# Kernel optimization log

Measured on AMD Instinct MI355X. Metric: run time of the kernel, lower is better.

## Reference

```python
import jax, jax.numpy as jnp
import numpy as np
import math

N_SAMPLES = 15


def sample_match(P, n_samples=N_SAMPLES):
    """Greedy argmax matching with row/col suppression, vectorized over batch.
    P: [B, N, M] (non-negative softmax scores). Returns (rows, cols): [B, S] int32.
    Matches torch: idx = (P == P.max()).nonzero()[0] -> first (row-major) argmax.
    """
    B, N, M = P.shape
    row_ids = jnp.arange(N)
    col_ids = jnp.arange(M)

    def step(P, _):
        flat_idx = jnp.argmax(P.reshape(B, N * M), axis=1)  # first max, row-major
        row = flat_idx // M  # [B]
        col = flat_idx % M   # [B]
        # suppress chosen row and column: P[row,:]=0 ; P[:,col]=0
        mask = (row_ids[None, :, None] == row[:, None, None]) | (
            col_ids[None, None, :] == col[:, None, None])  # [B,N,M]
        P = jnp.where(mask, jnp.zeros((), P.dtype), P)
        return P, (row, col)

    _, (rows, cols) = jax.lax.scan(step, P, None, length=n_samples)
    return rows.T, cols.T  # [B, S]


def setup_inputs() -> dict:
    key = jax.random.key(0)
    k1, k2, k3, k4 = jax.random.split(key, 4)
    B, D, N = 16, 512, 2048
    return {
        "src_embedding": jax.random.normal(k1, (B, D, N), dtype=jnp.float32),
        "tgt_embedding": jax.random.normal(k2, (B, D, N), dtype=jnp.float32),
        "src": jax.random.normal(k3, (B, N, 3), dtype=jnp.float32),
        "tgt": jax.random.normal(k4, (B, N, 3), dtype=jnp.float32),
    }


def reference(src_embedding, tgt_embedding, src, tgt):
    # input_shape == 'bnc': permute point clouds to [B, 3, N]
    src = jnp.swapaxes(src, 1, 2)
    tgt = jnp.swapaxes(tgt, 1, 2)
    B = src.shape[0]
    d_k = src_embedding.shape[1]

    # scores[b, s, t] = softmax_t( <src_emb[b,:,s], tgt_emb[b,:,t]> / sqrt(d_k) )
    logits = jnp.einsum('bds,bdt->bst', src_embedding, tgt_embedding) / math.sqrt(d_k)
    scores = jax.nn.softmax(logits, axis=2)

    # greedy one-to-one matching on detached scores
    rows, cols = sample_match(jax.lax.stop_gradient(scores))  # [B, S]

    # gather matched points: [B, 3, S]
    topk_src = jnp.take_along_axis(src, rows[:, None, :], axis=2)
    topk_tgt = jnp.take_along_axis(tgt, cols[:, None, :], axis=2)

    src_c = topk_src - topk_src.mean(axis=2, keepdims=True)
    tgt_c = topk_tgt - topk_tgt.mean(axis=2, keepdims=True)
    H = jnp.einsum('bis,bjs->bij', src_c, tgt_c)  # [B, 3, 3]

    u, s, vh = jnp.linalg.svd(H)
    v = jnp.swapaxes(vh, -1, -2)  # torch.svd returns V, jnp returns V^H
    ut = jnp.swapaxes(u, -1, -2)
    r = v @ ut
    det = jnp.linalg.det(r)
    reflect = jnp.array([1.0, 1.0, -1.0], dtype=H.dtype)  # diag(1,1,-1) right-mult
    r_fix = (v * reflect[None, None, :]) @ ut
    R = jnp.where((det < 0)[:, None, None], r_fix, r)  # [B, 3, 3]

    # soft correspondence: src_corr = tgt @ scores^T  -> [B, 3, N_src]
    src_corr = jnp.einsum('bjt,bst->bjs', tgt, scores)
    t = jnp.einsum('bij,bj->bi', -R, src.mean(axis=2)) + src_corr.mean(axis=2)
    return R, t.reshape(B, 3)
```

## Files before the change

kernel.cpp:

```cpp
#include <hip/hip_runtime.h>
#include <hip/hip_fp16.h>
#include <math.h>

typedef unsigned short u16;
typedef __attribute__((ext_vector_type(8))) short bf16x8;
typedef __attribute__((ext_vector_type(4))) float f32x4;

constexpr int B_ = 16;
constexpr int D_ = 512;
constexpr int N_ = 2048;
constexpr int S_ = 15;
constexpr int TOPK = 16;

constexpr int BK  = 32;
constexpr int KP  = 2 * D_;
constexpr int SCW = 132;
constexpr int BN7 = 256;
constexpr int NCH7 = N_ / BN7;

__device__ __forceinline__ void gl_lds16(const void* g, void* s) {
    __builtin_amdgcn_global_load_lds(
        (const __attribute__((address_space(1))) unsigned int*)g,
        (__attribute__((address_space(3))) unsigned int*)s, 16, 0, 0);
}

__device__ __forceinline__ unsigned enc1(float x) {
    x = fminf(x, 448.f);
    unsigned u = __float_as_uint(x);
    if (u < 0x3C800000u) return 0u;
    unsigned r = u + 0x7FFFFu + ((u >> 20) & 1u);
    unsigned f = (r >> 20) - 0x3C0u;
    return f > 0x7Eu ? 0x7Eu : f;
}
__device__ __forceinline__ float dec1(unsigned f) {
    return f ? __uint_as_float((f + 0x3C0u) << 20) : 0.f;
}

__global__ __launch_bounds__(256) void packbf(
    const float* __restrict__ srcE, const float* __restrict__ tgtE,
    u16* __restrict__ srcP, u16* __restrict__ tgtP)
{
    const int t = threadIdx.x;
    const int b = blockIdx.z & 15, sel = blockIdx.z >> 4;
    const float* in = (sel ? tgtE : srcE) + (size_t)b * D_ * N_;
    u16* out = (sel ? tgtP : srcP) + (size_t)b * N_ * KP;
    const int n0 = blockIdx.x * 64, k0 = blockIdx.y * 64;

    __shared__ float T[64][69];

    #pragma unroll
    for (int it = 0; it < 4; it++) {
        int r = it * 16 + (t >> 4);
        int c = (t & 15) * 4;
        float4 v = *(const float4*)&in[(size_t)(k0 + r) * N_ + n0 + c];
        T[c + 0][r] = v.x; T[c + 1][r] = v.y; T[c + 2][r] = v.z; T[c + 3][r] = v.w;
    }
    __syncthreads();

    const int nn = t >> 2, kc = (t & 3) * 16;
    __align__(16) u16 hi[16], lo[16];
    #pragma unroll
    for (int j = 0; j < 16; j++) {
        float x = T[nn][kc + j];
        unsigned u = __float_as_uint(x);
        unsigned hr = u + 0x7fff + ((u >> 16) & 1);
        u16 h = (u16)(hr >> 16);
        float hf = __uint_as_float((unsigned)h << 16);
        float xl = x - hf;
        unsigned ul = __float_as_uint(xl);
        unsigned lr = ul + 0x7fff + ((ul >> 16) & 1);
        hi[j] = h; lo[j] = (u16)(lr >> 16);
    }
    u16* op = out + (size_t)(n0 + nn) * KP + k0 + kc;
    *(int4*)op         = *(int4*)hi;  *(int4*)(op + 8)   = *(int4*)(hi + 8);
    *(int4*)(op + 512) = *(int4*)lo;  *(int4*)(op + 520) = *(int4*)(lo + 8);
}

__global__ __launch_bounds__(512, 2) void gemm7(
    const u16* __restrict__ srcP, const u16* __restrict__ tgtP,
    float* __restrict__ rzbuf, float* __restrict__ topv, int* __restrict__ topc,
    unsigned char* __restrict__ e8)
{
    __shared__ __align__(16) u16 sS[2 * 16384];
    __shared__ __align__(16) float sC[128 * SCW];

    const int tid = threadIdx.x;
    const int w = tid >> 6, lane = tid & 63;
    const int wr = w >> 2, wc = w & 3;
    const int sr = lane >> 2, q = lane & 3;
    const int bid = blockIdx.x;
    const int swz = (bid & 7) * 32 + (bid >> 3);
    const int b  = swz >> 4;
    const int s0 = (swz & 15) * 128;
    const float scale = 0.044194173824159216f;

    const u16* srcPb = srcP + (size_t)b * N_ * KP;
    const u16* tgtPb = tgtP + (size_t)b * N_ * KP;

    const int sls = ((lane & 3) ^ ((lane >> 3) & 3)) * 8;
    const u16* pAh = srcPb + (size_t)(s0 + w * 16 + (lane >> 2)) * KP + sls;
    const u16* pB  = tgtPb + (size_t)(w * 16 + (lane >> 2)) * KP + sls;
    const int aro = (lane & 15) * BK + (((lane >> 4) ^ ((lane >> 1) & 3)) * 8);

    auto stage = [&](int bi, int s, int c0) {
        u16* base = &sS[bi * 16384];
        const int t32 = (s & 15) * BK;
        gl_lds16(pAh + t32, base + w * 512);
        if (s < 16) {
            gl_lds16(pAh + 512 + t32, base + 4096 + w * 512);
            gl_lds16(pB + (size_t)c0 * KP + t32,         base + 8192 + w * 512);
            gl_lds16(pB + (size_t)(c0 + 128) * KP + t32, base + 12288 + w * 512);
        } else {
            gl_lds16(pB + (size_t)c0 * KP + 512 + t32,         base + 8192 + w * 512);
            gl_lds16(pB + (size_t)(c0 + 128) * KP + 512 + t32, base + 12288 + w * 512);
        }
    };

    float z_loc = 0.f;
    float tv[TOPK]; int tc16[TOPK];
    #pragma unroll
    for (int k = 0; k < TOPK; k++) { tv[k] = -1e30f; tc16[k] = 0x7fffffff; }

    stage(0, 0, 0);

    for (int ch = 0; ch < NCH7; ch++) {
        const int c0 = ch * BN7;
        f32x4 acc[4][4];
        #pragma unroll
        for (int i = 0; i < 4; i++)
            #pragma unroll
            for (int j = 0; j < 4; j++) acc[i][j] = (f32x4){0.f, 0.f, 0.f, 0.f};

        for (int s = 0; s < 32; s++) {
            __syncthreads();
            if (s < 31)              stage((s + 1) & 1, s + 1, c0);
            else if (ch < NCH7 - 1)  stage(0, 0, c0 + BN7);
            const u16* base = &sS[(s & 1) * 16384];
            bf16x8 afr[4], bfr[4];
            #pragma unroll
            for (int j = 0; j < 4; j++)
                bfr[j] = *(const bf16x8*)&base[8192 + wc * 2048 + j * 512 + aro];
            #pragma unroll
            for (int i = 0; i < 4; i++)
                afr[i] = *(const bf16x8*)&base[wr * 2048 + i * 512 + aro];
            #pragma unroll
            for (int i = 0; i < 4; i++)
                #pragma unroll
                for (int j = 0; j < 4; j++)
                    acc[i][j] = __builtin_amdgcn_mfma_f32_16x16x32_bf16(
                        afr[i], bfr[j], acc[i][j], 0, 0, 0);
            if (s < 16) {
                #pragma unroll
                for (int i = 0; i < 4; i++)
                    afr[i] = *(const bf16x8*)&base[4096 + wr * 2048 + i * 512 + aro];
                #pragma unroll
                for (int i = 0; i < 4; i++)
                    #pragma unroll
                    for (int j = 0; j < 4; j++)
                        acc[i][j] = __builtin_amdgcn_mfma_f32_16x16x32_bf16(
                            afr[i], bfr[j], acc[i][j], 0, 0, 0);
            }
        }

        #pragma unroll 1
        for (int h = 0; h < 2; h++) {
            __syncthreads();
            if ((wc >> 1) == h) {
                const int cb = (wc & 1) * 64;
                #pragma unroll
                for (int i = 0; i < 4; i++)
                    #pragma unroll
                    for (int j = 0; j < 4; j++)
                        #pragma unroll
                        for (int r = 0; r < 4; r++)
                            sC[(wr * 64 + i * 16 + (lane >> 4) * 4 + r) * SCW
                               + cb + j * 16 + (lane & 15)] = acc[i][j][r] * scale;
            }
            __syncthreads();
            const float* rowp = &sC[(w * 16 + sr) * SCW + q * 32];
            const int cbase = c0 + h * 128 + q * 32;
            const size_t erow = ((size_t)(b * N_ + s0 + w * 16 + sr)) * N_
                                + c0 + h * 128 + q * 32;
            #pragma unroll 1
            for (int mo = 0; mo < 2; mo++) {
                unsigned ow0 = 0, ow1 = 0, ow2 = 0, ow3 = 0;
                #pragma unroll
                for (int mi = 0; mi < 4; mi++) {
                    float4 v4 = *(const float4*)&rowp[mo * 16 + mi * 4];
                    const float vv[4] = {v4.x, v4.y, v4.z, v4.w};
                    unsigned wb = 0;
                    #pragma unroll
                    for (int e = 0; e < 4; e++) {
                        float v = vv[e];
                        float ex = __expf(v);
                        z_loc += ex;
                        wb |= enc1(ex) << (8 * e);
                        if (v > tv[15]) {
                            const int c = cbase + mo * 16 + mi * 4 + e;
                            #pragma unroll
                            for (int k = 15; k >= 1; k--) {
                                bool bk  = v > tv[k];
                                bool bk1 = v > tv[k - 1];
                                float sv = bk1 ? tv[k - 1] : v;
                                int   sc = bk1 ? tc16[k - 1] : c;
                                tv[k]   = bk ? sv : tv[k];
                                tc16[k] = bk ? sc : tc16[k];
                            }
                            if (v > tv[0]) { tv[0] = v; tc16[0] = c; }
                        }
                    }
                    if (mi == 0) ow0 = wb; else if (mi == 1) ow1 = wb;
                    else if (mi == 2) ow2 = wb; else ow3 = wb;
                }
                if (e8) *(uint4*)&e8[erow + mo * 16] = make_uint4(ow0, ow1, ow2, ow3);
            }
        }
    }

    float* sCw = &sC[w * 16 * SCW];
    int*   cbw = (int*)sCw;
    float* vbw = sCw + 1024;
    float* zqw = sCw + 2048;
    zqw[lane] = z_loc;
    #pragma unroll
    for (int k = 0; k < TOPK; k++) {
        vbw[lane * 16 + k] = tv[k];
        cbw[lane * 16 + k] = tc16[k];
    }
    if (q == 0) {
        float Z = zqw[lane] + zqw[lane + 1] + zqw[lane + 2] + zqw[lane + 3];
        float lz = logf(Z);
        const int grow = s0 + w * 16 + sr;
        rzbuf[b * N_ + grow] = 1.0f / Z;
        float tmin = -1e30f; int tminslot = 0, tmincol = 0x7fffffff;
        #pragma unroll
        for (int k = 0; k < TOPK; k++) { tv[k] = -1e30f; tc16[k] = 0x7fffffff; }
        for (int qq = 0; qq < 4; qq++) {
            #pragma unroll 1
            for (int k = 0; k < TOPK; k++) {
                float v = vbw[(lane + qq) * 16 + k];
                int c = cbw[(lane + qq) * 16 + k];
                bool ins = (v > tmin) || (v == tmin && c < tmincol);
                if (ins) {
                    #pragma unroll
                    for (int k2 = 0; k2 < TOPK; k2++)
                        if (k2 == tminslot) { tv[k2] = v; tc16[k2] = c; }
                    tmin = tv[0]; tmincol = tc16[0]; tminslot = 0;
                    #pragma unroll
                    for (int k2 = 1; k2 < TOPK; k2++) {
                        bool worse = (tv[k2] < tmin) || (tv[k2] == tmin && tc16[k2] > tmincol);
                        if (worse) { tmin = tv[k2]; tmincol = tc16[k2]; tminslot = k2; }
                    }
                }
            }
        }
        unsigned used = 0;
        size_t rowbase = ((size_t)b * N_ + grow) * TOPK;
        for (int o = 0; o < TOPK; o++) {
            float bvv = -1e31f; int bcc = 0x7fffffff; int bk = 0;
            #pragma unroll
            for (int k = 0; k < TOPK; k++) {
                bool u = (used >> k) & 1u;
                bool better = !u && ((tv[k] > bvv) || (tv[k] == bvv && tc16[k] < bcc));
                if (better) { bvv = tv[k]; bcc = tc16[k]; bk = k; }
            }
            used |= 1u << bk;
            topv[rowbase + o] = bvv - lz;
            topc[rowbase + o] = bcc;
        }
    }
}

__global__ __launch_bounds__(256) void colsum3(
    const unsigned char* __restrict__ e8, const float* __restrict__ rzbuf,
    float* __restrict__ colsum)
{
    const int b = blockIdx.z, s0 = blockIdx.y * 128, t0 = blockIdx.x * 1024;
    __shared__ float srz[128];
    if (threadIdx.x < 128) srz[threadIdx.x] = rzbuf[b * N_ + s0 + threadIdx.x];
    __syncthreads();
    const int t = t0 + threadIdx.x * 4;
    const unsigned char* p = e8 + ((size_t)(b * N_ + s0)) * N_ + t;
    float a0 = 0.f, a1 = 0.f, a2 = 0.f, a3 = 0.f;
    #pragma unroll 4
    for (int s = 0; s < 128; s++) {
        unsigned v = *(const unsigned*)(p + (size_t)s * N_);
        float r = srz[s];
        a0 += dec1(v & 255u) * r;
        a1 += dec1((v >> 8) & 255u) * r;
        a2 += dec1((v >> 16) & 255u) * r;
        a3 += dec1(v >> 24) * r;
    }
    atomicAdd(&colsum[b * N_ + t + 0], a0);
    atomicAdd(&colsum[b * N_ + t + 1], a1);
    atomicAdd(&colsum[b * N_ + t + 2], a2);
    atomicAdd(&colsum[b * N_ + t + 3], a3);
}

__global__ __launch_bounds__(512, 2) void gemm8(
    const u16* __restrict__ srcP, const u16* __restrict__ tgtP,
    const float* __restrict__ rzbuf, float* __restrict__ colsum)
{
    __shared__ __align__(16) u16 sS[2 * 16384];
    __shared__ float sRZ[128];

    const int tid = threadIdx.x;
    const int w = tid >> 6, lane = tid & 63;
    const int wr = w >> 2, wc = w & 3;
    const int bid = blockIdx.x;
    const int swz = (bid & 7) * 64 + (bid >> 3);
    const int b   = swz >> 5;
    const int rb  = swz & 31;
    const int s0  = (rb & 15) * 128;
    const int cb0 = (rb >> 4) * 1024;
    const float scale = 0.044194173824159216f;

    const u16* srcPb = srcP + (size_t)b * N_ * KP;
    const u16* tgtPb = tgtP + (size_t)b * N_ * KP;

    if (tid < 128) sRZ[tid] = rzbuf[b * N_ + s0 + tid];

    const int sls = ((lane & 3) ^ ((lane >> 3) & 3)) * 8;
    const u16* pAh = srcPb + (size_t)(s0 + w * 16 + (lane >> 2)) * KP + sls;
    const u16* pB  = tgtPb + (size_t)(w * 16 + (lane >> 2)) * KP + sls;
    const int aro = (lane & 15) * BK + (((lane >> 4) ^ ((lane >> 1) & 3)) * 8);

    auto stage = [&](int bi, int s, int c0) {
        u16* base = &sS[bi * 16384];
        const int t32 = (s & 15) * BK;
        gl_lds16(pAh + t32, base + w * 512);
        if (s < 16) {
            gl_lds16(pAh + 512 + t32, base + 4096 + w * 512);
            gl_lds16(pB + (size_t)c0 * KP + t32,         base + 8192 + w * 512);
            gl_lds16(pB + (size_t)(c0 + 128) * KP + t32, base + 12288 + w * 512);
        } else {
            gl_lds16(pB + (size_t)c0 * KP + 512 + t32,         base + 8192 + w * 512);
            gl_lds16(pB + (size_t)(c0 + 128) * KP + 512 + t32, base + 12288 + w * 512);
        }
    };

    stage(0, 0, cb0);

    for (int ch = 0; ch < 4; ch++) {
        const int c0 = cb0 + ch * BN7;
        f32x4 acc[4][4];
        #pragma unroll
        for (int i = 0; i < 4; i++)
            #pragma unroll
            for (int j = 0; j < 4; j++) acc[i][j] = (f32x4){0.f, 0.f, 0.f, 0.f};

        for (int s = 0; s < 32; s++) {
            __syncthreads();
            if (s < 31)      stage((s + 1) & 1, s + 1, c0);
            else if (ch < 3) stage(0, 0, c0 + BN7);
            const u16* base = &sS[(s & 1) * 16384];
            bf16x8 afr[4], bfr[4];
            #pragma unroll
            for (int j = 0; j < 4; j++)
                bfr[j] = *(const bf16x8*)&base[8192 + wc * 2048 + j * 512 + aro];
            #pragma unroll
            for (int i = 0; i < 4; i++)
                afr[i] = *(const bf16x8*)&base[wr * 2048 + i * 512 + aro];
            #pragma unroll
            for (int i = 0; i < 4; i++)
                #pragma unroll
                for (int j = 0; j < 4; j++)
                    acc[i][j] = __builtin_amdgcn_mfma_f32_16x16x32_bf16(
                        afr[i], bfr[j], acc[i][j], 0, 0, 0);
            if (s < 16) {
                #pragma unroll
                for (int i = 0; i < 4; i++)
                    afr[i] = *(const bf16x8*)&base[4096 + wr * 2048 + i * 512 + aro];
                #pragma unroll
                for (int i = 0; i < 4; i++)
                    #pragma unroll
                    for (int j = 0; j < 4; j++)
                        acc[i][j] = __builtin_amdgcn_mfma_f32_16x16x32_bf16(
                            afr[i], bfr[j], acc[i][j], 0, 0, 0);
            }
        }

        #pragma unroll
        for (int j = 0; j < 4; j++) {
            float s = 0.f;
            #pragma unroll
            for (int i = 0; i < 4; i++)
                #pragma unroll
                for (int r = 0; r < 4; r++)
                    s += __expf(acc[i][j][r] * scale)
                         * sRZ[wr * 64 + i * 16 + (lane >> 4) * 4 + r];
            s += __shfl_xor(s, 16);
            s += __shfl_xor(s, 32);
            if (lane < 16)
                atomicAdd(&colsum[b * N_ + c0 + wc * 64 + j * 16 + lane], s);
        }
    }
}

__global__ __launch_bounds__(256) void match2(
    const float* __restrict__ topv, const int* __restrict__ topc,
    int* __restrict__ mrow, int* __restrict__ mcol)
{
    const int b = blockIdx.x, tid = threadIdx.x;
    __shared__ float bv[N_];
    __shared__ int bc[N_];
    __shared__ int sup[16];
    __shared__ float rv[256];
    __shared__ int rr[256];

    for (int r = tid; r < N_; r += 256) {
        bv[r] = topv[((size_t)b * N_ + r) * TOPK];
        bc[r] = topc[((size_t)b * N_ + r) * TOPK];
    }
    __syncthreads();

    for (int it = 0; it < S_; it++) {
        float mv = -1e30f; int mr = 0x7fffffff;
        #pragma unroll
        for (int j = 0; j < 8; j++) {
            int r = tid + j * 256;
            float v = bv[r];
            if (v > mv) { mv = v; mr = r; }
        }
        rv[tid] = mv; rr[tid] = mr;
        __syncthreads();
        for (int off = 128; off; off >>= 1) {
            if (tid < off) {
                float v2 = rv[tid + off];
                if (v2 > rv[tid] || (v2 == rv[tid] && rr[tid + off] < rr[tid])) {
                    rv[tid] = v2; rr[tid] = rr[tid + off];
                }
            }
            __syncthreads();
        }
        if (tid == 0) {
            int R = rr[0]; int C = bc[R];
            mrow[b * S_ + it] = R; mcol[b * S_ + it] = C;
            sup[it] = C;
            bv[R] = -1e30f;
        }
        __syncthreads();
        const int C = sup[it];
        for (int r = tid; r < N_; r += 256) {
            if (bc[r] == C && bv[r] > -1e29f) {
                float nv = -1e30f; int nc = 0x7fffffff;
                const float* tvp = &topv[((size_t)b * N_ + r) * TOPK];
                const int* tcp = &topc[((size_t)b * N_ + r) * TOPK];
                for (int k = 0; k < TOPK; k++) {
                    int c2 = tcp[k];
                    bool bad = false;
                    for (int qq = 0; qq <= it; qq++) bad = bad || (sup[qq] == c2);
                    if (!bad) { nv = tvp[k]; nc = c2; break; }
                }
                bv[r] = nv; bc[r] = nc;
            }
        }
        __syncthreads();
    }
}

__global__ void finish_kernel(const float* __restrict__ src,
                              const float* __restrict__ tgt,
                              const float* __restrict__ colsum,
                              const int* __restrict__ mrow,
                              const int* __restrict__ mcol,
                              float* __restrict__ out)
{
    const int b = blockIdx.x;
    const int tid = threadIdx.x;
    __shared__ float red[256];
    __shared__ float res[6];

    float ls[3] = {0, 0, 0}, lc[3] = {0, 0, 0};
    for (int n = tid; n < N_; n += 256) {
        float cs = colsum[b * N_ + n];
        #pragma unroll
        for (int j = 0; j < 3; j++) {
            ls[j] += src[(size_t)(b * N_ + n) * 3 + j];
            lc[j] += tgt[(size_t)(b * N_ + n) * 3 + j] * cs;
        }
    }
    for (int j = 0; j < 6; j++) {
        red[tid] = (j < 3) ? ls[j] : lc[j - 3];
        __syncthreads();
        for (int off = 128; off; off >>= 1) {
            if (tid < off) red[tid] += red[tid + off];
            __syncthreads();
        }
        if (tid == 0) res[j] = red[0] / (float)N_;
        __syncthreads();
    }

    if (tid == 0) {
        double ps[S_][3], pt[S_][3];
        double ms[3] = {0, 0, 0}, mt[3] = {0, 0, 0};
        for (int s = 0; s < S_; s++) {
            int r = mrow[b * S_ + s], c = mcol[b * S_ + s];
            for (int j = 0; j < 3; j++) {
                ps[s][j] = (double)src[(size_t)(b * N_ + r) * 3 + j];
                pt[s][j] = (double)tgt[(size_t)(b * N_ + c) * 3 + j];
                ms[j] += ps[s][j]; mt[j] += pt[s][j];
            }
        }
        for (int j = 0; j < 3; j++) { ms[j] /= S_; mt[j] /= S_; }
        double H[3][3] = {{0,0,0},{0,0,0},{0,0,0}};
        for (int s = 0; s < S_; s++)
            for (int i = 0; i < 3; i++)
                for (int j = 0; j < 3; j++)
                    H[i][j] += (ps[s][i] - ms[i]) * (pt[s][j] - mt[j]);

        double A[3][3], Vv[3][3] = {{1,0,0},{0,1,0},{0,0,1}};
        for (int i = 0; i < 3; i++)
            for (int j = 0; j < 3; j++) {
                double acc = 0;
                for (int k = 0; k < 3; k++) acc += H[k][i] * H[k][j];
                A[i][j] = acc;
            }
        for (int sweep = 0; sweep < 30; sweep++) {
            double off = fabs(A[0][1]) + fabs(A[0][2]) + fabs(A[1][2]);
            if (off < 1e-30) break;
            for (int pair = 0; pair < 3; pair++) {
                int p = (pair == 2) ? 1 : 0;
                int q = (pair == 0) ? 1 : 2;
                double apq = A[p][q];
                if (fabs(apq) < 1e-300) continue;
                double theta = (A[q][q] - A[p][p]) / (2.0 * apq);
                double tt = ((theta >= 0) ? 1.0 : -1.0) / (fabs(theta) + sqrt(theta * theta + 1.0));
                double cc = 1.0 / sqrt(tt * tt + 1.0);
                double ssn = tt * cc;
                for (int k = 0; k < 3; k++) {
                    double akp = A[k][p], akq = A[k][q];
                    A[k][p] = cc * akp - ssn * akq;
                    A[k][q] = ssn * akp + cc * akq;
                }
                for (int k = 0; k < 3; k++) {
                    double apk = A[p][k], aqk = A[q][k];
                    A[p][k] = cc * apk - ssn * aqk;
                    A[q][k] = ssn * apk + cc * aqk;
                }
                for (int k = 0; k < 3; k++) {
                    double vkp = Vv[k][p], vkq = Vv[k][q];
                    Vv[k][p] = cc * vkp - ssn * vkq;
                    Vv[k][q] = ssn * vkp + cc * vkq;
                }
            }
        }
        double wv[3] = {A[0][0], A[1][1], A[2][2]};
        for (int a = 0; a < 2; a++)
            for (int b2 = a + 1; b2 < 3; b2++)
                if (wv[b2] > wv[a]) {
                    double tw = wv[a]; wv[a] = wv[b2]; wv[b2] = tw;
                    for (int k = 0; k < 3; k++) {
                        double tv_ = Vv[k][a]; Vv[k][a] = Vv[k][b2]; Vv[k][b2] = tv_;
                    }
                }
        double U[3][3];
        for (int k = 0; k < 3; k++) {
            double u[3], nrm = 0;
            for (int i = 0; i < 3; i++) {
                double acc = 0;
                for (int j = 0; j < 3; j++) acc += H[i][j] * Vv[j][k];
                u[i] = acc; nrm += acc * acc;
            }
            nrm = sqrt(nrm);
            if (nrm < 1e-300) nrm = 1e-300;
            for (int i = 0; i < 3; i++) U[i][k] = u[i] / nrm;
        }
        double r[3][3];
        for (int i = 0; i < 3; i++)
            for (int j = 0; j < 3; j++) {
                double acc = 0;
                for (int k = 0; k < 3; k++) acc += Vv[i][k] * U[j][k];
                r[i][j] = acc;
            }
        double det = r[0][0] * (r[1][1] * r[2][2] - r[1][2] * r[2][1])
                   - r[0][1] * (r[1][0] * r[2][2] - r[1][2] * r[2][0])
                   + r[0][2] * (r[1][0] * r[2][1] - r[1][1] * r[2][0]);
        if (det < 0.0) {
            for (int i = 0; i < 3; i++)
                for (int j = 0; j < 3; j++)
                    r[i][j] -= 2.0 * Vv[i][2] * U[j][2];
        }
        double smean[3] = {(double)res[0], (double)res[1], (double)res[2]};
        double cmean[3] = {(double)res[3], (double)res[4], (double)res[5]};
        for (int i = 0; i < 3; i++)
            for (int j = 0; j < 3; j++)
                out[b * 9 + i * 3 + j] = (float)r[i][j];
        for (int i = 0; i < 3; i++) {
            double acc = cmean[i];
            for (int j = 0; j < 3; j++) acc -= r[i][j] * smean[j];
            out[B_ * 9 + b * 3 + i] = (float)acc;
        }
    }
}

extern "C" void kernel_launch(void* const* d_in, const int* in_sizes, int n_in,
                              void* d_out, int out_size, void* d_ws, size_t ws_size,
                              hipStream_t stream)
{
    const float* srcE = (const float*)d_in[0];
    const float* tgtE = (const float*)d_in[1];
    const float* src  = (const float*)d_in[2];
    const float* tgt  = (const float*)d_in[3];
    float* out = (float*)d_out;
    char* ws = (char*)d_ws;

    const size_t szP  = (size_t)B_ * N_ * KP * sizeof(u16);
    const size_t szE8 = (size_t)B_ * N_ * N_;
    const size_t szStats = (size_t)B_ * N_ * sizeof(float)
                         + (size_t)B_ * N_ * TOPK * sizeof(float)
                         + (size_t)B_ * N_ * TOPK * sizeof(int)
                         + (size_t)B_ * N_ * sizeof(float)
                         + 2048;
    const bool fat = ws_size >= 2 * szP + szE8 + szStats;

    u16* srcP = (u16*)ws;
    u16* tgtP = (u16*)(ws + szP);
    unsigned char* e8 = fat ? (unsigned char*)(ws + 2 * szP) : nullptr;
    size_t off = 2 * szP + (fat ? szE8 : 0);
    float* rzbuf  = (float*)(ws + off); off += (size_t)B_ * N_ * sizeof(float);
    float* topv   = (float*)(ws + off); off += (size_t)B_ * N_ * TOPK * sizeof(float);
    int*   topc   = (int*)(ws + off);   off += (size_t)B_ * N_ * TOPK * sizeof(int);
    float* colsum = (float*)(ws + off); off += (size_t)B_ * N_ * sizeof(float);
    int*   mrow   = (int*)(ws + off);   off += 1024;
    int*   mcol   = (int*)(ws + off);

    hipMemsetAsync(colsum, 0, (size_t)B_ * N_ * sizeof(float), stream);

    packbf<<<dim3(N_ / 64, D_ / 64, 2 * B_), 256, 0, stream>>>(srcE, tgtE, srcP, tgtP);
    gemm7<<<dim3(256), 512, 0, stream>>>(srcP, tgtP, rzbuf, topv, topc, e8);
    if (fat)
        colsum3<<<dim3(2, 16, 16), 256, 0, stream>>>(e8, rzbuf, colsum);
    else
        gemm8<<<dim3(512), 512, 0, stream>>>(srcP, tgtP, rzbuf, colsum);
    match2<<<B_, 256, 0, stream>>>(topv, topc, mrow, mcol);
    finish_kernel<<<B_, 256, 0, stream>>>(src, tgt, colsum, mrow, mcol, out);
}
```

Before: 712.0 us.

## Triple-buffer GEMM LDS stages with distance-two prefetch and manual vmcnt waits

The GEMM main loop moves from a double-buffered LDS scheme with __syncthreads to a three-buffer ring. Loads are issued two steps ahead and gated by explicit s_waitcnt vmcnt counts plus raw s_barrier, so global-to-LDS loads overlap more MFMA work and barriers no longer drain all outstanding loads. To fit the extra buffer, the softmax/top-k epilogue staging area shrinks to a 64-column tile processed in four passes instead of two. The cost is more epilogue barriers, a full vmcnt drain at the end of each chunk, and fragile hand-tuned wait counts that must match the loads and stores actually in flight.

```diff
diff --git a/kernel.cpp b/kernel.cpp
--- a/kernel.cpp
+++ b/kernel.cpp
@@ -14,9 +14,8 @@
 
 constexpr int BK  = 32;
 constexpr int KP  = 2 * D_;
-constexpr int SCW = 132;
 constexpr int BN7 = 256;
-constexpr int NCH7 = N_ / BN7;
+constexpr int SCW4 = 68;
 
 __device__ __forceinline__ void gl_lds16(const void* g, void* s) {
     __builtin_amdgcn_global_load_lds(
@@ -81,8 +80,8 @@
     float* __restrict__ rzbuf, float* __restrict__ topv, int* __restrict__ topc,
     unsigned char* __restrict__ e8)
 {
-    __shared__ __align__(16) u16 sS[2 * 16384];
-    __shared__ __align__(16) float sC[128 * SCW];
+    __shared__ __align__(16) u16 sS[3 * 16384];
+    __shared__ __align__(16) float sC[128 * SCW4];
 
     const int tid = threadIdx.x;
     const int w = tid >> 6, lane = tid & 63;
@@ -102,11 +101,13 @@
     const u16* pB  = tgtPb + (size_t)(w * 16 + (lane >> 2)) * KP + sls;
     const int aro = (lane & 15) * BK + (((lane >> 4) ^ ((lane >> 1) & 3)) * 8);
 
-    auto stage = [&](int bi, int s, int c0) {
+    auto stageG = [&](int bi, int g) {
         u16* base = &sS[bi * 16384];
-        const int t32 = (s & 15) * BK;
+        const int st = g & 31;
+        const int c0 = (g >> 5) * BN7;
+        const int t32 = (st & 15) * BK;
         gl_lds16(pAh + t32, base + w * 512);
-        if (s < 16) {
+        if (st < 16) {
             gl_lds16(pAh + 512 + t32, base + 4096 + w * 512);
             gl_lds16(pB + (size_t)c0 * KP + t32,         base + 8192 + w * 512);
             gl_lds16(pB + (size_t)(c0 + 128) * KP + t32, base + 12288 + w * 512);
@@ -121,10 +122,11 @@
     #pragma unroll
     for (int k = 0; k < TOPK; k++) { tv[k] = -1e30f; tc16[k] = 0x7fffffff; }
 
-    stage(0, 0, 0);
-
-    for (int ch = 0; ch < NCH7; ch++) {
-        const int c0 = ch * BN7;
+    stageG(0, 0);
+    stageG(1, 1);
+    int bi = 0, bi2 = 2;
+
+    for (int ch = 0; ch < 8; ch++) {
         f32x4 acc[4][4];
         #pragma unroll
         for (int i = 0; i < 4; i++)
@@ -132,10 +134,14 @@
             for (int j = 0; j < 4; j++) acc[i][j] = (f32x4){0.f, 0.f, 0.f, 0.f};
 
         for (int s = 0; s < 32; s++) {
-            __syncthreads();
-            if (s < 31)              stage((s + 1) & 1, s + 1, c0);
-            else if (ch < NCH7 - 1)  stage(0, 0, c0 + BN7);
-            const u16* base = &sS[(s & 1) * 16384];
+            const int g = ch * 32 + s;
+            if (g == 255)                 asm volatile("s_waitcnt vmcnt(0)" ::: "memory");
+            else if (((g + 1) & 31) < 16) asm volatile("s_waitcnt vmcnt(4)" ::: "memory");
+            else                          asm volatile("s_waitcnt vmcnt(3)" ::: "memory");
+            __builtin_amdgcn_s_barrier();
+            __builtin_amdgcn_sched_barrier(0);
+            if (g + 2 < 256) stageG(bi2, g + 2);
+            const u16* base = &sS[bi * 16384];
             bf16x8 afr[4], bfr[4];
             #pragma unroll
             for (int j = 0; j < 4; j++)
@@ -160,64 +166,67 @@
                         acc[i][j] = __builtin_amdgcn_mfma_f32_16x16x32_bf16(
                             afr[i], bfr[j], acc[i][j], 0, 0, 0);
             }
-        }
-
+            bi  = (bi  == 2) ? 0 : bi + 1;
+            bi2 = (bi2 == 2) ? 0 : bi2 + 1;
+        }
+
+        const int c0 = ch * BN7;
         #pragma unroll 1
-        for (int h = 0; h < 2; h++) {
-            __syncthreads();
-            if ((wc >> 1) == h) {
-                const int cb = (wc & 1) * 64;
+        for (int h = 0; h < 4; h++) {
+            asm volatile("s_waitcnt lgkmcnt(0)" ::: "memory");
+            __builtin_amdgcn_s_barrier();
+            if (wc == h) {
                 #pragma unroll
                 for (int i = 0; i < 4; i++)
                     #pragma unroll
                     for (int j = 0; j < 4; j++)
                         #pragma unroll
                         for (int r = 0; r < 4; r++)
-                            sC[(wr * 64 + i * 16 + (lane >> 4) * 4 + r) * SCW
-                               + cb + j * 16 + (lane & 15)] = acc[i][j][r] * scale;
-            }
-            __syncthreads();
-            const float* rowp = &sC[(w * 16 + sr) * SCW + q * 32];
-            const int cbase = c0 + h * 128 + q * 32;
-            const size_t erow = ((size_t)(b * N_ + s0 + w * 16 + sr)) * N_
-                                + c0 + h * 128 + q * 32;
-            #pragma unroll 1
-            for (int mo = 0; mo < 2; mo++) {
-                unsigned ow0 = 0, ow1 = 0, ow2 = 0, ow3 = 0;
-                #pragma unroll
-                for (int mi = 0; mi < 4; mi++) {
-                    float4 v4 = *(const float4*)&rowp[mo * 16 + mi * 4];
-                    const float vv[4] = {v4.x, v4.y, v4.z, v4.w};
-                    unsigned wb = 0;
-                    #pragma unroll
-                    for (int e = 0; e < 4; e++) {
-                        float v = vv[e];
-                        float ex = __expf(v);
-                        z_loc += ex;
-                        wb |= enc1(ex) << (8 * e);
-                        if (v > tv[15]) {
-                            const int c = cbase + mo * 16 + mi * 4 + e;
-                            #pragma unroll
-                            for (int k = 15; k >= 1; k--) {
-                                bool bk  = v > tv[k];
-                                bool bk1 = v > tv[k - 1];
-                                float sv = bk1 ? tv[k - 1] : v;
-                                int   sc = bk1 ? tc16[k - 1] : c;
-                                tv[k]   = bk ? sv : tv[k];
-                                tc16[k] = bk ? sc : tc16[k];
-                            }
-                            if (v > tv[0]) { tv[0] = v; tc16[0] = c; }
+                            sC[(wr * 64 + i * 16 + (lane >> 4) * 4 + r) * SCW4
+                               + j * 16 + (lane & 15)] = acc[i][j][r] * scale;
+            }
+            asm volatile("s_waitcnt lgkmcnt(0)" ::: "memory");
+            __builtin_amdgcn_s_barrier();
+            const float* rowp = &sC[(w * 16 + sr) * SCW4 + q * 16];
+            const int cbase = c0 + h * 64 + q * 16;
+            unsigned ow0 = 0, ow1 = 0, ow2 = 0, ow3 = 0;
+            #pragma unroll
+            for (int mi = 0; mi < 4; mi++) {
+                float4 v4 = *(const float4*)&rowp[mi * 4];
+                const float vv[4] = {v4.x, v4.y, v4.z, v4.w};
+                unsigned wb = 0;
+                #pragma unroll
+                for (int e = 0; e < 4; e++) {
+                    float v = vv[e];
+                    float ex = __expf(v);
+                    z_loc += ex;
+                    wb |= enc1(ex) << (8 * e);
+                    if (v > tv[15]) {
+                        const int c = cbase + mi * 4 + e;
+                        #pragma unroll
+                        for (int k = 15; k >= 1; k--) {
+                            bool bk  = v > tv[k];
+                            bool bk1 = v > tv[k - 1];
+                            float sv = bk1 ? tv[k - 1] : v;
+                            int   sc = bk1 ? tc16[k - 1] : c;
+                            tv[k]   = bk ? sv : tv[k];
+                            tc16[k] = bk ? sc : tc16[k];
                         }
+                        if (v > tv[0]) { tv[0] = v; tc16[0] = c; }
                     }
-                    if (mi == 0) ow0 = wb; else if (mi == 1) ow1 = wb;
-                    else if (mi == 2) ow2 = wb; else ow3 = wb;
-                }
-                if (e8) *(uint4*)&e8[erow + mo * 16] = make_uint4(ow0, ow1, ow2, ow3);
-            }
-        }
-    }
-
-    float* sCw = &sC[w * 16 * SCW];
+                }
+                if (mi == 0) ow0 = wb; else if (mi == 1) ow1 = wb;
+                else if (mi == 2) ow2 = wb; else ow3 = wb;
+            }
+            if (e8) {
+                const size_t erow = ((size_t)(b * N_ + s0 + w * 16 + sr)) * N_ + cbase;
+                *(uint4*)&e8[erow] = make_uint4(ow0, ow1, ow2, ow3);
+            }
+        }
+        asm volatile("s_waitcnt vmcnt(0)" ::: "memory");
+    }
+
+    float* sCw = (float*)sS + w * 2112;
     int*   cbw = (int*)sCw;
     float* vbw = sCw + 1024;
     float* zqw = sCw + 2048;
```

Result: slower. 803.9 us (+12.9%).
